# Optimization experiments

Measured on AMD Instinct MI355X. Metric: run time of the kernel, lower is better.

The kernel has to match this reference:

```python
import jax, jax.numpy as jnp
import numpy as np

B, C, H, W = 4, 256, 48, 48
NUM_HEADS = 8
HEAD_DIM = C // NUM_HEADS
LN_EPS = 1e-5


def setup_inputs() -> dict:
    key = jax.random.key(0)
    ks = jax.random.split(key, 12)
    s = 1.0 / np.sqrt(C)
    return {
        "x": jax.random.normal(ks[0], (B, C, H, W), dtype=jnp.float32),
        "context": jax.random.normal(ks[1], (B, C, H, W), dtype=jnp.float32),
        "Wq": jax.random.uniform(ks[2], (C, C), jnp.float32, -s, s),
        "bq": jax.random.uniform(ks[3], (C,), jnp.float32, -s, s),
        "Wk": jax.random.uniform(ks[4], (C, C), jnp.float32, -s, s),
        "bk": jax.random.uniform(ks[5], (C,), jnp.float32, -s, s),
        "Wv": jax.random.uniform(ks[6], (C, C), jnp.float32, -s, s),
        "bv": jax.random.uniform(ks[7], (C,), jnp.float32, -s, s),
        "Wo": jax.random.uniform(ks[8], (C, C), jnp.float32, -s, s),
        "bo": jax.random.uniform(ks[9], (C,), jnp.float32, -s, s),
        "ln_w": jnp.ones((C,), jnp.float32),
        "ln_b": jnp.zeros((C,), jnp.float32),
    }


def reference(x, context, Wq, bq, Wk, bk, Wv, bv, Wo, bo, ln_w, ln_b):
    b, c, h, w = x.shape
    S = h * w
    # [B, S, C] token layout (x.view(B,C,-1).permute(0,2,1))
    x_flat = x.reshape(b, c, S).transpose(0, 2, 1)
    ctx_flat = context.reshape(b, c, S).transpose(0, 2, 1)
    # QKV projections (torch Linear: y = x @ W.T + b)
    q = (x_flat @ Wq.T + bq).reshape(b, S, NUM_HEADS, HEAD_DIM).transpose(0, 2, 1, 3)
    k = (ctx_flat @ Wk.T + bk).reshape(b, S, NUM_HEADS, HEAD_DIM).transpose(0, 2, 1, 3)
    v = (ctx_flat @ Wv.T + bv).reshape(b, S, NUM_HEADS, HEAD_DIM).transpose(0, 2, 1, 3)
    # attention: [B, heads, S, S]
    scores = jnp.einsum("bhqd,bhkd->bhqk", q, k) / np.sqrt(HEAD_DIM)
    attn = jax.nn.softmax(scores, axis=-1)  # dropout is identity in eval mode
    attended = jnp.einsum("bhqk,bhkd->bhqd", attn, v)
    attended = attended.transpose(0, 2, 1, 3).reshape(b, S, c)
    out = attended @ Wo.T + bo
    # residual + layernorm over channel dim
    y = out + x_flat
    mu = jnp.mean(y, axis=-1, keepdims=True)
    var = jnp.var(y, axis=-1, keepdims=True)
    y = (y - mu) * jax.lax.rsqrt(var + LN_EPS) * ln_w + ln_b
    return y.transpose(0, 2, 1).reshape(b, c, h, w)
```

## Files before the change

### kernel.cpp

```cpp
#include <hip/hip_runtime.h>

#define B_ 4
#define C_ 256
#define S_ 2304
#define NH_ 8
#define HD_ 32
#define QS_L2E (0.17677669529663687f * 1.4426950408889634f)

typedef __attribute__((ext_vector_type(8))) __bf16 b16x8;
typedef __attribute__((ext_vector_type(4))) __bf16 b16x4;
typedef __attribute__((ext_vector_type(4))) float f32x4;
typedef __attribute__((ext_vector_type(4))) unsigned u32x4;

static __device__ __forceinline__ f32x4 mfma_bf16(b16x8 a, b16x8 b, f32x4 c) {
  return __builtin_amdgcn_mfma_f32_16x16x32_bf16(a, b, c, 0, 0, 0);
}

__global__ __launch_bounds__(256) void k_cvtw(
    const float* __restrict__ Wq, const float* __restrict__ Wk,
    const float* __restrict__ Wv, const float* __restrict__ Wo,
    __bf16* __restrict__ Wb, __bf16* __restrict__ Wob) {
  const int e = blockIdx.x * 1024 + threadIdx.x * 4;
  const float* s;
  __bf16* d;
  if (e < 196608) {
    const int m = e >> 16;
    s = (m == 0 ? Wq : (m == 1 ? Wk : Wv)) + (e & 65535);
    d = Wb + e;
  } else {
    s = Wo + (e - 196608);
    d = Wob + (e - 196608);
  }
  f32x4 v = *(const f32x4*)s;
  b16x4 o;
#pragma unroll
  for (int j = 0; j < 4; ++j) o[j] = (__bf16)v[j];
  *(b16x4*)d = o;
}

__global__ __launch_bounds__(256) void k_qkv(
    const float* __restrict__ x, const float* __restrict__ ctx,
    const __bf16* __restrict__ Wb,
    const float* __restrict__ bq, const float* __restrict__ bk, const float* __restrict__ bv,
    __bf16* __restrict__ Q, __bf16* __restrict__ Kd, __bf16* __restrict__ Vt) {
  __shared__ __bf16 lx[33][264];
  const int t = threadIdx.x;
  const int iblk = t >> 6;
  const int lane = t & 63;
  const int col = lane & 15, g = lane >> 4;
  int r = blockIdx.x;
  const int p = r / 288; r %= 288;
  const int b = r / 72;
  const int s0 = (r % 72) * 32;
  const float* src = (p == 0 ? x : ctx) + (size_t)b * C_ * S_ + s0;
  const __bf16* W = Wb + p * 65536;
  const float* bias = p == 0 ? bq : (p == 1 ? bk : bv);
  const int i0 = iblk * 64;
  const __bf16* arow = W + (size_t)(i0 + col) * C_ + g * 8;

  b16x8 af0 = *(const b16x8*)(arow);
  b16x8 af1 = *(const b16x8*)(arow + (size_t)16 * C_);
  b16x8 af2 = *(const b16x8*)(arow + (size_t)32 * C_);
  b16x8 af3 = *(const b16x8*)(arow + (size_t)48 * C_);

  {
    const int tr = t >> 3, tc = (t & 7) * 4;
#pragma unroll
    for (int j = 0; j < 8; ++j) {
      const int c = j * 32 + tr;
      f32x4 v = *(const f32x4*)(src + (size_t)c * S_ + tc);
#pragma unroll
      for (int jj = 0; jj < 4; ++jj) lx[tc + jj][c] = (__bf16)v[jj];
    }
  }
  __syncthreads();

  f32x4 acc[2][4] = {};
  b16x8 bf0 = *(const b16x8*)(&lx[col][g * 8]);
  b16x8 bf1 = *(const b16x8*)(&lx[16 + col][g * 8]);

  for (int kk = 0; kk < 8; ++kk) {
    const int nk = ((kk + 1) & 7) * 32;
    b16x8 nbf0 = *(const b16x8*)(&lx[col][nk + g * 8]);
    b16x8 nbf1 = *(const b16x8*)(&lx[16 + col][nk + g * 8]);
    b16x8 naf0 = *(const b16x8*)(arow + nk);
    b16x8 naf1 = *(const b16x8*)(arow + (size_t)16 * C_ + nk);
    b16x8 naf2 = *(const b16x8*)(arow + (size_t)32 * C_ + nk);
    b16x8 naf3 = *(const b16x8*)(arow + (size_t)48 * C_ + nk);
    __builtin_amdgcn_sched_barrier(0);
    acc[0][0] = mfma_bf16(af0, bf0, acc[0][0]);
    acc[0][1] = mfma_bf16(af1, bf0, acc[0][1]);
    acc[0][2] = mfma_bf16(af2, bf0, acc[0][2]);
    acc[0][3] = mfma_bf16(af3, bf0, acc[0][3]);
    acc[1][0] = mfma_bf16(af0, bf1, acc[1][0]);
    acc[1][1] = mfma_bf16(af1, bf1, acc[1][1]);
    acc[1][2] = mfma_bf16(af2, bf1, acc[1][2]);
    acc[1][3] = mfma_bf16(af3, bf1, acc[1][3]);
    bf0 = nbf0; bf1 = nbf1; af0 = naf0; af1 = naf1; af2 = naf2; af3 = naf3;
  }
#pragma unroll
  for (int tf = 0; tf < 2; ++tf) {
#pragma unroll
    for (int j = 0; j < 4; ++j) {
#pragma unroll
      for (int rr = 0; rr < 4; ++rr) {
        const int i = i0 + j * 16 + g * 4 + rr;
        float val = acc[tf][j][rr] + bias[i];
        const int h = i >> 5, d = i & 31;
        const size_t bh = (size_t)b * NH_ + h;
        const int tok = s0 + tf * 16 + col;
        if (p == 0)      Q[(bh * S_ + tok) * HD_ + d] = (__bf16)(val * QS_L2E);
        else if (p == 1) Kd[(bh * S_ + tok) * HD_ + d] = (__bf16)val;
        else             Vt[(bh * HD_ + d) * S_ + tok] = (__bf16)val;
      }
    }
  }
}

__global__ __launch_bounds__(256) void k_attn(
    const __bf16* __restrict__ Q, const __bf16* __restrict__ Kd,
    const __bf16* __restrict__ Vt, __bf16* __restrict__ att) {
  __shared__ float mrg[3][4][528];
  int bid = blockIdx.x;
  bid = (bid & 7) * 144 + (bid >> 3);
  const int wid = threadIdx.x >> 6;
  const int lane = threadIdx.x & 63;
  const int col = lane & 15, g = lane >> 4;
  const int bh = bid / 36;
  const int s0 = (bid % 36) * 64;
  const int b = bh >> 3, h = bh & 7;
  const __bf16* Qb = Q + (size_t)bh * S_ * HD_;
  const __bf16* Kb = Kd + (size_t)bh * S_ * HD_;
  const __bf16* Vb = Vt + (size_t)bh * HD_ * S_;

  b16x8 qfr[4];
#pragma unroll
  for (int q = 0; q < 4; ++q)
    qfr[q] = *(const b16x8*)(Qb + (size_t)(s0 + q * 16 + col) * HD_ + g * 8);
  const int kA = ((col >> 2) * 8) + (col & 3);
  const int kbeg = wid * (S_ / 4);

  b16x8 onesf;
#pragma unroll
  for (int j = 0; j < 8; ++j) onesf[j] = (__bf16)1.0f;

  f32x4 acc0[4] = {}, acc1[4] = {}, accl[4] = {};
  const f32x4 zero = {};

  const __bf16* kptr = Kb + (size_t)(kbeg + kA) * HD_ + g * 8;
  const __bf16* vptr = Vb + (size_t)col * S_ + kbeg + g * 8;

  b16x8 ka = *(const b16x8*)(kptr);
  b16x8 kb = *(const b16x8*)(kptr + 4 * HD_);
  b16x8 v0 = *(const b16x8*)(vptr);
  b16x8 v1 = *(const b16x8*)(vptr + 16 * S_);

  for (int it = 0; it < S_ / 4 / 32; ++it) {
    kptr += 32 * HD_; vptr += 32;
    b16x8 ka_n = *(const b16x8*)(kptr);
    b16x8 kb_n = *(const b16x8*)(kptr + 4 * HD_);
    b16x8 v0_n = *(const b16x8*)(vptr);
    b16x8 v1_n = *(const b16x8*)(vptr + 16 * S_);
    __builtin_amdgcn_sched_barrier(0);

#pragma unroll
    for (int q = 0; q < 4; ++q) {
      f32x4 sA = mfma_bf16(ka, qfr[q], zero);
      f32x4 sB = mfma_bf16(kb, qfr[q], zero);
      float eA0 = __builtin_amdgcn_exp2f(sA[0]);
      float eA1 = __builtin_amdgcn_exp2f(sA[1]);
      float eA2 = __builtin_amdgcn_exp2f(sA[2]);
      float eA3 = __builtin_amdgcn_exp2f(sA[3]);
      float eB0 = __builtin_amdgcn_exp2f(sB[0]);
      float eB1 = __builtin_amdgcn_exp2f(sB[1]);
      float eB2 = __builtin_amdgcn_exp2f(sB[2]);
      float eB3 = __builtin_amdgcn_exp2f(sB[3]);
      unsigned w0, w1, w2, w3;
      asm("v_cvt_pk_bf16_f32 %0, %1, %2" : "=v"(w0) : "v"(eA0), "v"(eA1));
      asm("v_cvt_pk_bf16_f32 %0, %1, %2" : "=v"(w1) : "v"(eA2), "v"(eA3));
      asm("v_cvt_pk_bf16_f32 %0, %1, %2" : "=v"(w2) : "v"(eB0), "v"(eB1));
      asm("v_cvt_pk_bf16_f32 %0, %1, %2" : "=v"(w3) : "v"(eB2), "v"(eB3));
      u32x4 pw = {w0, w1, w2, w3};
      b16x8 pf = __builtin_bit_cast(b16x8, pw);
      acc0[q] = mfma_bf16(pf, v0, acc0[q]);
      acc1[q] = mfma_bf16(pf, v1, acc1[q]);
      accl[q] = mfma_bf16(pf, onesf, accl[q]);
    }
    ka = ka_n; kb = kb_n; v0 = v0_n; v1 = v1_n;
  }

  if (wid > 0) {
#pragma unroll
    for (int qt = 0; qt < 4; ++qt) {
      float* m0 = mrg[wid - 1][qt];
      *(f32x4*)(m0 + col * 16 + g * 4) = acc0[qt];
      *(f32x4*)(m0 + (col + 16) * 16 + g * 4) = acc1[qt];
      if (col == 0) *(f32x4*)(m0 + 512 + g * 4) = accl[qt];
    }
  }
  __syncthreads();
  if (wid == 0) {
#pragma unroll
    for (int qt = 0; qt < 4; ++qt) {
      f32x4 t0 = acc0[qt], t1 = acc1[qt], tl = accl[qt];
#pragma unroll
      for (int m = 0; m < 3; ++m) {
        const float* pm = mrg[m][qt];
        t0 += *(const f32x4*)(pm + col * 16 + g * 4);
        t1 += *(const f32x4*)(pm + (col + 16) * 16 + g * 4);
        tl += *(const f32x4*)(pm + 512 + g * 4);
      }
#pragma unroll
      for (int j = 0; j < 4; ++j) {
        const int q = g * 4 + j;
        const float inv = 1.f / tl[j];
        const size_t obase = ((size_t)b * S_ + s0 + qt * 16 + q) * C_ + h * HD_;
        att[obase + col] = (__bf16)(t0[j] * inv);
        att[obase + 16 + col] = (__bf16)(t1[j] * inv);
      }
    }
  }
}

__global__ __launch_bounds__(256) void k_oln(
    const __bf16* __restrict__ att, const __bf16* __restrict__ Wob,
    const float* __restrict__ bo, const float* __restrict__ x,
    const float* __restrict__ lnw, const float* __restrict__ lnb,
    float* __restrict__ out) {
  __shared__ float part[4][2][16];
  __shared__ float lw[256], lb[256];
  const int wid = threadIdx.x >> 6;
  const int lane = threadIdx.x & 63;
  const int col = lane & 15, g = lane >> 4;
  int r = blockIdx.x;
  const int b = r / 144;
  const int s0 = (r % 144) * 16;
  const int i0 = wid * 64;
  lw[threadIdx.x] = lnw[threadIdx.x];
  lb[threadIdx.x] = lnb[threadIdx.x];

  f32x4 acc[4] = {};
  const __bf16* arow = att + ((size_t)b * S_ + s0 + col) * C_ + g * 8;
  const __bf16* wrow = Wob + (size_t)(i0 + col) * C_ + g * 8;

  b16x8 bfr = *(const b16x8*)(arow);
  b16x8 af0 = *(const b16x8*)(wrow);
  b16x8 af1 = *(const b16x8*)(wrow + (size_t)16 * C_);
  b16x8 af2 = *(const b16x8*)(wrow + (size_t)32 * C_);
  b16x8 af3 = *(const b16x8*)(wrow + (size_t)48 * C_);

  for (int kk = 0; kk < 8; ++kk) {
    const int nk = ((kk + 1) & 7) * 32;
    b16x8 nbfr = *(const b16x8*)(arow + nk);
    b16x8 naf0 = *(const b16x8*)(wrow + nk);
    b16x8 naf1 = *(const b16x8*)(wrow + (size_t)16 * C_ + nk);
    b16x8 naf2 = *(const b16x8*)(wrow + (size_t)32 * C_ + nk);
    b16x8 naf3 = *(const b16x8*)(wrow + (size_t)48 * C_ + nk);
    __builtin_amdgcn_sched_barrier(0);
    acc[0] = mfma_bf16(af0, bfr, acc[0]);
    acc[1] = mfma_bf16(af1, bfr, acc[1]);
    acc[2] = mfma_bf16(af2, bfr, acc[2]);
    acc[3] = mfma_bf16(af3, bfr, acc[3]);
    bfr = nbfr; af0 = naf0; af1 = naf1; af2 = naf2; af3 = naf3;
  }
  float s = 0.f, s2 = 0.f;
#pragma unroll
  for (int j = 0; j < 4; ++j) {
#pragma unroll
    for (int rr = 0; rr < 4; ++rr) {
      const int i = i0 + j * 16 + g * 4 + rr;
      float v = acc[j][rr] + bo[i] + x[((size_t)b * C_ + i) * S_ + s0 + col];
      acc[j][rr] = v;
      s += v; s2 += v * v;
    }
  }
  s += __shfl_xor(s, 16); s2 += __shfl_xor(s2, 16);
  s += __shfl_xor(s, 32); s2 += __shfl_xor(s2, 32);
  if (g == 0) { part[wid][0][col] = s; part[wid][1][col] = s2; }
  __syncthreads();
  float st = part[0][0][col] + part[1][0][col] + part[2][0][col] + part[3][0][col];
  float st2 = part[0][1][col] + part[1][1][col] + part[2][1][col] + part[3][1][col];
  const float mu = st * (1.f / 256.f);
  const float rs = rsqrtf(st2 * (1.f / 256.f) - mu * mu + 1e-5f);
#pragma unroll
  for (int j = 0; j < 4; ++j) {
#pragma unroll
    for (int rr = 0; rr < 4; ++rr) {
      const int i = i0 + j * 16 + g * 4 + rr;
      out[((size_t)b * C_ + i) * S_ + s0 + col] = (acc[j][rr] - mu) * rs * lw[i] + lb[i];
    }
  }
}

extern "C" void kernel_launch(void* const* d_in, const int* in_sizes, int n_in,
                              void* d_out, int out_size, void* d_ws, size_t ws_size,
                              hipStream_t stream) {
  const float* x   = (const float*)d_in[0];
  const float* ctx = (const float*)d_in[1];
  const float* Wq  = (const float*)d_in[2];
  const float* bq  = (const float*)d_in[3];
  const float* Wk  = (const float*)d_in[4];
  const float* bk  = (const float*)d_in[5];
  const float* Wv  = (const float*)d_in[6];
  const float* bv  = (const float*)d_in[7];
  const float* Wo  = (const float*)d_in[8];
  const float* bo  = (const float*)d_in[9];
  const float* lnw = (const float*)d_in[10];
  const float* lnb = (const float*)d_in[11];
  float* out = (float*)d_out;

  char* ws = (char*)d_ws;
  __bf16* Wb  = (__bf16*)(ws + 9437184);
  __bf16* Wob = (__bf16*)(ws + 9830400);
  __bf16* Kd  = (__bf16*)(ws + 9961472);
  __bf16* Vt  = (__bf16*)(ws + 14680064);
  __bf16* att = (__bf16*)(ws + 19398656);
  __bf16* Q   = (__bf16*)(ws + 24117248);

  k_cvtw <<< 256, 256, 0, stream>>>(Wq, Wk, Wv, Wo, Wb, Wob);
  k_qkv  <<< 864, 256, 0, stream>>>(x, ctx, Wb, bq, bk, bv, Q, Kd, Vt);
  k_attn <<<1152, 256, 0, stream>>>(Q, Kd, Vt, att);
  k_oln  <<< 576, 256, 0, stream>>>(att, Wob, bo, x, lnw, lnb, out);
}
```

Measured before the change: 173.9 us.

## Halve token tiles in QKV and attention kernels, add occupancy hint and padded merge

Token tiles shrink from 32 to 16 in the QKV projection and from 64 to 32 queries in attention. This doubles the grid of each kernel and cuts register use per thread, and attention gains a launch_bounds occupancy hint of 7. The attention loop drops its explicit software prefetch and sched_barrier, and the merge buffer in shared memory is padded with a stride of 20 to avoid bank conflicts. QKV now loads bias as a vector and writes Q and K with vector stores. The trade-off is that each K/V element is loaded more times in total, and there is less latency hiding inside each wave.

```diff
diff --git a/kernel.cpp b/kernel.cpp
--- a/kernel.cpp
+++ b/kernel.cpp
@@ -43,19 +43,19 @@
     const __bf16* __restrict__ Wb,
     const float* __restrict__ bq, const float* __restrict__ bk, const float* __restrict__ bv,
     __bf16* __restrict__ Q, __bf16* __restrict__ Kd, __bf16* __restrict__ Vt) {
-  __shared__ __bf16 lx[33][264];
+  __shared__ __bf16 lx[16][264];
   const int t = threadIdx.x;
-  const int iblk = t >> 6;
+  const int wid = t >> 6;
   const int lane = t & 63;
   const int col = lane & 15, g = lane >> 4;
   int r = blockIdx.x;
-  const int p = r / 288; r %= 288;
-  const int b = r / 72;
-  const int s0 = (r % 72) * 32;
+  const int p = r / 576; r %= 576;
+  const int b = r / 144;
+  const int s0 = (r % 144) * 16;
   const float* src = (p == 0 ? x : ctx) + (size_t)b * C_ * S_ + s0;
   const __bf16* W = Wb + p * 65536;
   const float* bias = p == 0 ? bq : (p == 1 ? bk : bv);
-  const int i0 = iblk * 64;
+  const int i0 = wid * 64;
   const __bf16* arow = W + (size_t)(i0 + col) * C_ + g * 8;
 
   b16x8 af0 = *(const b16x8*)(arow);
@@ -64,78 +64,78 @@
   b16x8 af3 = *(const b16x8*)(arow + (size_t)48 * C_);
 
   {
-    const int tr = t >> 3, tc = (t & 7) * 4;
-#pragma unroll
-    for (int j = 0; j < 8; ++j) {
-      const int c = j * 32 + tr;
-      f32x4 v = *(const f32x4*)(src + (size_t)c * S_ + tc);
-#pragma unroll
-      for (int jj = 0; jj < 4; ++jj) lx[tc + jj][c] = (__bf16)v[jj];
+    const int cr = t >> 2, sq = (t & 3) * 4;
+#pragma unroll
+    for (int j = 0; j < 4; ++j) {
+      const int c = j * 64 + cr;
+      f32x4 v = *(const f32x4*)(src + (size_t)c * S_ + sq);
+#pragma unroll
+      for (int jj = 0; jj < 4; ++jj) lx[sq + jj][c] = (__bf16)v[jj];
     }
   }
   __syncthreads();
 
-  f32x4 acc[2][4] = {};
-  b16x8 bf0 = *(const b16x8*)(&lx[col][g * 8]);
-  b16x8 bf1 = *(const b16x8*)(&lx[16 + col][g * 8]);
+  f32x4 acc[4] = {};
+  b16x8 bf = *(const b16x8*)(&lx[col][g * 8]);
 
   for (int kk = 0; kk < 8; ++kk) {
     const int nk = ((kk + 1) & 7) * 32;
-    b16x8 nbf0 = *(const b16x8*)(&lx[col][nk + g * 8]);
-    b16x8 nbf1 = *(const b16x8*)(&lx[16 + col][nk + g * 8]);
+    b16x8 nbf = *(const b16x8*)(&lx[col][nk + g * 8]);
     b16x8 naf0 = *(const b16x8*)(arow + nk);
     b16x8 naf1 = *(const b16x8*)(arow + (size_t)16 * C_ + nk);
     b16x8 naf2 = *(const b16x8*)(arow + (size_t)32 * C_ + nk);
     b16x8 naf3 = *(const b16x8*)(arow + (size_t)48 * C_ + nk);
     __builtin_amdgcn_sched_barrier(0);
-    acc[0][0] = mfma_bf16(af0, bf0, acc[0][0]);
-    acc[0][1] = mfma_bf16(af1, bf0, acc[0][1]);
-    acc[0][2] = mfma_bf16(af2, bf0, acc[0][2]);
-    acc[0][3] = mfma_bf16(af3, bf0, acc[0][3]);
-    acc[1][0] = mfma_bf16(af0, bf1, acc[1][0]);
-    acc[1][1] = mfma_bf16(af1, bf1, acc[1][1]);
-    acc[1][2] = mfma_bf16(af2, bf1, acc[1][2]);
-    acc[1][3] = mfma_bf16(af3, bf1, acc[1][3]);
-    bf0 = nbf0; bf1 = nbf1; af0 = naf0; af1 = naf1; af2 = naf2; af3 = naf3;
-  }
-#pragma unroll
-  for (int tf = 0; tf < 2; ++tf) {
-#pragma unroll
-    for (int j = 0; j < 4; ++j) {
-#pragma unroll
-      for (int rr = 0; rr < 4; ++rr) {
-        const int i = i0 + j * 16 + g * 4 + rr;
-        float val = acc[tf][j][rr] + bias[i];
-        const int h = i >> 5, d = i & 31;
-        const size_t bh = (size_t)b * NH_ + h;
-        const int tok = s0 + tf * 16 + col;
-        if (p == 0)      Q[(bh * S_ + tok) * HD_ + d] = (__bf16)(val * QS_L2E);
-        else if (p == 1) Kd[(bh * S_ + tok) * HD_ + d] = (__bf16)val;
-        else             Vt[(bh * HD_ + d) * S_ + tok] = (__bf16)val;
-      }
-    }
-  }
-}
-
-__global__ __launch_bounds__(256) void k_attn(
+    acc[0] = mfma_bf16(af0, bf, acc[0]);
+    acc[1] = mfma_bf16(af1, bf, acc[1]);
+    acc[2] = mfma_bf16(af2, bf, acc[2]);
+    acc[3] = mfma_bf16(af3, bf, acc[3]);
+    bf = nbf; af0 = naf0; af1 = naf1; af2 = naf2; af3 = naf3;
+  }
+  const int tok = s0 + col;
+#pragma unroll
+  for (int j = 0; j < 4; ++j) {
+    const int ib = i0 + j * 16 + g * 4;
+    f32x4 bi = *(const f32x4*)(bias + ib);
+    const int h = ib >> 5, d0 = ib & 31;
+    const size_t bh = (size_t)b * NH_ + h;
+    if (p == 2) {
+#pragma unroll
+      for (int rr = 0; rr < 4; ++rr)
+        Vt[(bh * HD_ + d0 + rr) * S_ + tok] = (__bf16)(acc[j][rr] + bi[rr]);
+    } else if (p == 1) {
+      b16x4 o;
+#pragma unroll
+      for (int rr = 0; rr < 4; ++rr) o[rr] = (__bf16)(acc[j][rr] + bi[rr]);
+      *(b16x4*)(Kd + (bh * S_ + tok) * HD_ + d0) = o;
+    } else {
+      b16x4 o;
+#pragma unroll
+      for (int rr = 0; rr < 4; ++rr) o[rr] = (__bf16)((acc[j][rr] + bi[rr]) * QS_L2E);
+      *(b16x4*)(Q + (bh * S_ + tok) * HD_ + d0) = o;
+    }
+  }
+}
+
+__global__ __launch_bounds__(256, 7) void k_attn(
     const __bf16* __restrict__ Q, const __bf16* __restrict__ Kd,
     const __bf16* __restrict__ Vt, __bf16* __restrict__ att) {
-  __shared__ float mrg[3][4][528];
+  __shared__ float mrg[3][2][656];
   int bid = blockIdx.x;
-  bid = (bid & 7) * 144 + (bid >> 3);
+  bid = (bid & 7) * 288 + (bid >> 3);
   const int wid = threadIdx.x >> 6;
   const int lane = threadIdx.x & 63;
   const int col = lane & 15, g = lane >> 4;
-  const int bh = bid / 36;
-  const int s0 = (bid % 36) * 64;
+  const int bh = bid / 72;
+  const int s0 = (bid % 72) * 32;
   const int b = bh >> 3, h = bh & 7;
   const __bf16* Qb = Q + (size_t)bh * S_ * HD_;
   const __bf16* Kb = Kd + (size_t)bh * S_ * HD_;
   const __bf16* Vb = Vt + (size_t)bh * HD_ * S_;
 
-  b16x8 qfr[4];
-#pragma unroll
-  for (int q = 0; q < 4; ++q)
+  b16x8 qfr[2];
+#pragma unroll
+  for (int q = 0; q < 2; ++q)
     qfr[q] = *(const b16x8*)(Qb + (size_t)(s0 + q * 16 + col) * HD_ + g * 8);
   const int kA = ((col >> 2) * 8) + (col & 3);
   const int kbeg = wid * (S_ / 4);
@@ -144,27 +144,20 @@
 #pragma unroll
   for (int j = 0; j < 8; ++j) onesf[j] = (__bf16)1.0f;
 
-  f32x4 acc0[4] = {}, acc1[4] = {}, accl[4] = {};
+  f32x4 acc0[2] = {}, acc1[2] = {}, accl[2] = {};
   const f32x4 zero = {};
 
   const __bf16* kptr = Kb + (size_t)(kbeg + kA) * HD_ + g * 8;
   const __bf16* vptr = Vb + (size_t)col * S_ + kbeg + g * 8;
 
-  b16x8 ka = *(const b16x8*)(kptr);
-  b16x8 kb = *(const b16x8*)(kptr + 4 * HD_);
-  b16x8 v0 = *(const b16x8*)(vptr);
-  b16x8 v1 = *(const b16x8*)(vptr + 16 * S_);
-
   for (int it = 0; it < S_ / 4 / 32; ++it) {
+    b16x8 ka = *(const b16x8*)(kptr);
+    b16x8 kb = *(const b16x8*)(kptr + 4 * HD_);
+    b16x8 v0 = *(const b16x8*)(vptr);
+    b16x8 v1 = *(const b16x8*)(vptr + 16 * S_);
     kptr += 32 * HD_; vptr += 32;
-    b16x8 ka_n = *(const b16x8*)(kptr);
-    b16x8 kb_n = *(const b16x8*)(kptr + 4 * HD_);
-    b16x8 v0_n = *(const b16x8*)(vptr);
-    b16x8 v1_n = *(const b16x8*)(vptr + 16 * S_);
-    __builtin_amdgcn_sched_barrier(0);
-
-#pragma unroll
-    for (int q = 0; q < 4; ++q) {
+#pragma unroll
+    for (int q = 0; q < 2; ++q) {
       f32x4 sA = mfma_bf16(ka, qfr[q], zero);
       f32x4 sB = mfma_bf16(kb, qfr[q], zero);
       float eA0 = __builtin_amdgcn_exp2f(sA[0]);
@@ -186,29 +179,28 @@
       acc1[q] = mfma_bf16(pf, v1, acc1[q]);
       accl[q] = mfma_bf16(pf, onesf, accl[q]);
     }
-    ka = ka_n; kb = kb_n; v0 = v0_n; v1 = v1_n;
   }
 
   if (wid > 0) {
 #pragma unroll
-    for (int qt = 0; qt < 4; ++qt) {
+    for (int qt = 0; qt < 2; ++qt) {
       float* m0 = mrg[wid - 1][qt];
-      *(f32x4*)(m0 + col * 16 + g * 4) = acc0[qt];
-      *(f32x4*)(m0 + (col + 16) * 16 + g * 4) = acc1[qt];
-      if (col == 0) *(f32x4*)(m0 + 512 + g * 4) = accl[qt];
+      *(f32x4*)(m0 + col * 20 + g * 4) = acc0[qt];
+      *(f32x4*)(m0 + 320 + col * 20 + g * 4) = acc1[qt];
+      if (col == 0) *(f32x4*)(m0 + 640 + g * 4) = accl[qt];
     }
   }
   __syncthreads();
   if (wid == 0) {
 #pragma unroll
-    for (int qt = 0; qt < 4; ++qt) {
+    for (int qt = 0; qt < 2; ++qt) {
       f32x4 t0 = acc0[qt], t1 = acc1[qt], tl = accl[qt];
 #pragma unroll
       for (int m = 0; m < 3; ++m) {
         const float* pm = mrg[m][qt];
-        t0 += *(const f32x4*)(pm + col * 16 + g * 4);
-        t1 += *(const f32x4*)(pm + (col + 16) * 16 + g * 4);
-        tl += *(const f32x4*)(pm + 512 + g * 4);
+        t0 += *(const f32x4*)(pm + col * 20 + g * 4);
+        t1 += *(const f32x4*)(pm + 320 + col * 20 + g * 4);
+        tl += *(const f32x4*)(pm + 640 + g * 4);
       }
 #pragma unroll
       for (int j = 0; j < 4; ++j) {
@@ -318,7 +310,7 @@
   __bf16* Q   = (__bf16*)(ws + 24117248);
 
   k_cvtw <<< 256, 256, 0, stream>>>(Wq, Wk, Wv, Wo, Wb, Wob);
-  k_qkv  <<< 864, 256, 0, stream>>>(x, ctx, Wb, bq, bk, bv, Q, Kd, Vt);
-  k_attn <<<1152, 256, 0, stream>>>(Q, Kd, Vt, att);
+  k_qkv  <<<1728, 256, 0, stream>>>(x, ctx, Wb, bq, bk, bv, Q, Kd, Vt);
+  k_attn <<<2304, 256, 0, stream>>>(Q, Kd, Vt, att);
   k_oln  <<< 576, 256, 0, stream>>>(att, Wob, bo, x, lnw, lnb, out);
 }
```

Measured after the change: 226.4 us. 30.2% more time.
